# Kernel optimization log

Measured on AMD Instinct MI355X. Metric: run time of the kernel, lower is better.

Reference implementation:

```python
import jax, jax.numpy as jnp
import numpy as np

H = 128; L = 3; ODIM = 400; SCALE = 30.0

def gather_nodes(h, E_idx):
    # h: [B,N,C], E_idx: [B,N,K] -> [B,N,K,C]
    B, N, K = E_idx.shape
    C = h.shape[-1]
    idx = jnp.broadcast_to(E_idx.reshape(B, N * K, 1), (B, N * K, C))
    return jnp.take_along_axis(h, idx, axis=1).reshape(B, N, K, C)

def layer_norm(x, eps=1e-5):
    mu = jnp.mean(x, axis=-1, keepdims=True)
    var = jnp.mean((x - mu) ** 2, axis=-1, keepdims=True)
    return (x - mu) / jnp.sqrt(var + eps)

def merge_dups(h_E, inv_mapping):
    # h_E: [B,N,K,C]; inv_mapping: [B,N*K]
    B, N, K, C = h_E.shape
    flat = h_E.reshape(B, N * K, C)
    idx = jnp.broadcast_to(inv_mapping[:, :, None], (B, N * K, C))
    return jnp.take_along_axis(flat, idx, axis=1).reshape(B, N, K, C)

def setup_inputs() -> dict:
    key = jax.random.key(0)
    ks = jax.random.split(key, 40)
    B, N, K = 2, 1024, 30
    d = {}
    d['h_V0'] = jax.random.normal(ks[0], (B, N, H), jnp.float32)
    d['h_E0'] = jax.random.normal(ks[1], (B, N, K, H), jnp.float32)
    d['E_idx'] = jax.random.randint(ks[2], (B, N, K), 0, N, jnp.int32)
    d['inv_mapping'] = jax.random.randint(ks[3], (B, N * K), 0, N * K, jnp.int32)
    d['x_mask'] = jnp.ones((B, N), jnp.float32)
    s = 0.05
    d['Wv_w'] = jax.random.normal(ks[4], (H, H)) * s; d['Wv_b'] = jnp.zeros((H,))
    d['We_w'] = jax.random.normal(ks[5], (H, H)) * s; d['We_b'] = jnp.zeros((H,))
    # node MPNN layers: message MLP (3h->h->h->h) + dense FFN (h->4h->h), stacked [L,...]
    d['nW1'] = jax.random.normal(ks[6], (L, 3 * H, H)) * s; d['nb1'] = jnp.zeros((L, H))
    d['nW2'] = jax.random.normal(ks[7], (L, H, H)) * s;     d['nb2'] = jnp.zeros((L, H))
    d['nW3'] = jax.random.normal(ks[8], (L, H, H)) * s;     d['nb3'] = jnp.zeros((L, H))
    d['nWd1'] = jax.random.normal(ks[9], (L, H, 4 * H)) * s; d['nbd1'] = jnp.zeros((L, 4 * H))
    d['nWd2'] = jax.random.normal(ks[10], (L, 4 * H, H)) * s; d['nbd2'] = jnp.zeros((L, H))
    # edge MPNN layers
    d['eW1'] = jax.random.normal(ks[11], (L, 3 * H, H)) * s; d['eb1'] = jnp.zeros((L, H))
    d['eW2'] = jax.random.normal(ks[12], (L, H, H)) * s;     d['eb2'] = jnp.zeros((L, H))
    d['eW3'] = jax.random.normal(ks[13], (L, H, H)) * s;     d['eb3'] = jnp.zeros((L, H))
    d['eWd1'] = jax.random.normal(ks[14], (L, H, 4 * H)) * s; d['ebd1'] = jnp.zeros((L, 4 * H))
    d['eWd2'] = jax.random.normal(ks[15], (L, 4 * H, H)) * s; d['ebd2'] = jnp.zeros((L, H))
    d['Wout_w'] = jax.random.normal(ks[16], (H, ODIM)) * s; d['Wout_b'] = jnp.zeros((ODIM,))
    return d

def reference(h_V0, h_E0, E_idx, inv_mapping, x_mask,
              Wv_w, Wv_b, We_w, We_b,
              nW1, nb1, nW2, nb2, nW3, nb3, nWd1, nbd1, nWd2, nbd2,
              eW1, eb1, eW2, eb2, eW3, eb3, eWd1, ebd1, eWd2, ebd2,
              Wout_w, Wout_b):
    B, N, K = E_idx.shape
    h_V = h_V0 @ Wv_w + Wv_b                      # W_v embedding
    h_E = h_E0 @ We_w + We_b                      # W_e embedding
    mask_attend = gather_nodes(x_mask[..., None], E_idx)[..., 0] * x_mask[..., None]  # [B,N,K]
    for l in range(L):
        # ---- node update (NodeMPNNLayer) ----
        h_nb = gather_nodes(h_V, E_idx)                           # [B,N,K,H]
        h_i = jnp.broadcast_to(h_V[:, :, None, :], h_nb.shape)
        h_EV = jnp.concatenate([h_i, h_nb, h_E], axis=-1)         # [B,N,K,3H]
        m = jax.nn.relu(h_EV @ nW1[l] + nb1[l])
        m = jax.nn.relu(m @ nW2[l] + nb2[l])
        m = m @ nW3[l] + nb3[l]
        m = m * mask_attend[..., None]
        dh = jnp.sum(m, axis=-2) / SCALE
        h_V = layer_norm(h_V + dh)
        dh = jax.nn.relu(h_V @ nWd1[l] + nbd1[l]) @ nWd2[l] + nbd2[l]
        h_V = layer_norm(h_V + dh)
        h_V = h_V * x_mask[..., None]
        # ---- edge update (EdgeMPNNLayer) ----
        h_j = gather_nodes(h_V, E_idx)
        h_i = jnp.broadcast_to(h_V[:, :, None, :], h_j.shape)
        h_EV = jnp.concatenate([h_i, h_E, h_j], axis=-1)          # [B,N,K,3H]
        m = jax.nn.relu(h_EV @ eW1[l] + eb1[l])
        m = jax.nn.relu(m @ eW2[l] + eb2[l])
        m = m @ eW3[l] + eb3[l]
        h_E = layer_norm(h_E + m)
        dh = jax.nn.relu(h_E @ eWd1[l] + ebd1[l]) @ eWd2[l] + ebd2[l]
        h_E = layer_norm(h_E + dh)
        h_E = h_E * mask_attend[..., None]
    etab = h_E @ Wout_w + Wout_b                                  # [B,N,K,400]
    etab = merge_dups(etab, inv_mapping)
    return etab
```

## Files before the change

### kernel.cpp

```cpp
#include <hip/hip_runtime.h>
#include <hip/hip_bf16.h>
#include <stdint.h>


typedef __bf16 bf16_t;
typedef __attribute__((ext_vector_type(8))) __bf16 bf16x8;
typedef __attribute__((ext_vector_type(4))) float f32x4;

#define B_    2
#define N_    1024
#define KN    30
#define H_    128
#define L_    3
#define ODIM_ 400
#define NK    (N_ * KN)
#define RT    (B_ * N_ * KN)
#define BN_   (B_ * N_)

#define EPI_PLAIN 0
#define EPI_RELU  1
#define EPI_F32   2
#define EPI_LN    4
#define EPI_OUT   5

__device__ __forceinline__ float wred(float v) {
#pragma unroll
  for (int off = 32; off > 0; off >>= 1) v += __shfl_xor(v, off, 64);
  return v;
}

__device__ __forceinline__ void gld16(const bf16_t* g, bf16_t* l) {
  __builtin_amdgcn_global_load_lds(
      (__attribute__((address_space(1))) void*)(g),
      (__attribute__((address_space(3))) void*)(l), 16, 0, 0);
}

__device__ __forceinline__ void barL() {
  asm volatile("s_waitcnt lgkmcnt(0)" ::: "memory");
  __builtin_amdgcn_s_barrier();
  __builtin_amdgcn_sched_barrier(0);
}
__device__ __forceinline__ void wait_v4_bar() {
  asm volatile("s_waitcnt vmcnt(4) lgkmcnt(0)" ::: "memory");
  __builtin_amdgcn_s_barrier();
  __builtin_amdgcn_sched_barrier(0);
}
__device__ __forceinline__ void wait_v0_bar() {
  asm volatile("s_waitcnt vmcnt(0) lgkmcnt(0)" ::: "memory");
  __builtin_amdgcn_s_barrier();
  __builtin_amdgcn_sched_barrier(0);
}

template<int NI>
__device__ __forceinline__ void mmN(const bf16_t* __restrict__ Ah,
                                    const bf16_t* __restrict__ Bh,
                                    int wm, int wn, int fm, int q, int fx,
                                    f32x4 (&acc)[4][NI])
{
#pragma unroll
  for (int h = 0; h < 2; ++h) {
    const int slot = ((((h << 2) | q) ^ fx) << 3);
    bf16x8 af[4], bfv[NI];
#pragma unroll
    for (int mi = 0; mi < 4; ++mi)
      af[mi] = *reinterpret_cast<const bf16x8*>(
          &Ah[(wm * 64 + mi * 16 + fm) * 64 + slot]);
#pragma unroll
    for (int ni = 0; ni < NI; ++ni)
      bfv[ni] = *reinterpret_cast<const bf16x8*>(
          &Bh[(wn * (NI * 16) + ni * 16 + fm) * 64 + slot]);
#pragma unroll
    for (int mi = 0; mi < 4; ++mi)
#pragma unroll
      for (int ni = 0; ni < NI; ++ni)
        acc[mi][ni] = __builtin_amdgcn_mfma_f32_16x16x32_bf16(
            af[mi], bfv[ni], acc[mi][ni], 0, 0, 0);
  }
}

struct GCArgs {
  const bf16_t* Ain;
  const bf16_t* W1; int koff1; int ldw1;
  const bf16_t* W2; const bf16_t* b2;
  const bf16_t* W3; const bf16_t* b3;
  const float* U; const float* G; const int* E;
  const float* ma;
  float* Agg;
  const bf16_t* Wd1; const bf16_t* bd1;
  const bf16_t* Wd2; const bf16_t* bd2;
  const float* mvec;
  bf16_t* outF;
  const bf16_t* Wug; const bf16_t* bug;
  float* Uo; float* Go;
};

template<int MODE>
__global__ __launch_bounds__(256, 2) void gc(GCArgs a)
{
  __shared__ __align__(16) bf16_t bufA[2][8192];
  __shared__ __align__(16) bf16_t bufB[2][8192];
  __shared__ __align__(16) bf16_t Ws[8192];
  float* lnS  = (float*)Ws;
  float* lnS2 = lnS + 256;
  float* aggS = (float*)Ws;

  const int tid = threadIdx.x;
  const int w = tid >> 6, l = tid & 63;
  const int wm = w & 1, wn = w >> 1;
  const int row0 = blockIdx.x * 128;
  const int lr = l >> 3;
  const int kg8 = ((l & 7) ^ lr) << 3;
  const int fm = l & 15, q = l >> 4, fx = fm & 7;

  auto stage128 = [&](const bf16_t* W, int ldw, int koff) {
    const bf16_t* gb = W + (size_t)(w * 32 + lr) * ldw + koff + kg8;
#pragma unroll
    for (int s = 0; s < 4; ++s)
      gld16(gb + (size_t)(s * 8) * ldw, &Ws[w * 2048 + s * 512]);
  };
  auto stageWd1 = [&](int c) {
    const bf16_t* gb = a.Wd1 + (size_t)(c * 64 + w * 16 + lr) * 128 + kg8;
#pragma unroll
    for (int s = 0; s < 2; ++s) {
      gld16(gb + (size_t)(s * 8) * 128,      &Ws[w * 1024 + s * 512]);
      gld16(gb + (size_t)(s * 8) * 128 + 64, &Ws[4096 + w * 1024 + s * 512]);
    }
  };
  auto stageWd2 = [&](int c) {
    const bf16_t* gb = a.Wd2 + (size_t)(w * 32 + lr) * 512 + c * 64 + kg8;
#pragma unroll
    for (int s = 0; s < 4; ++s)
      gld16(gb + (size_t)(s * 8) * 512, &bufA[1][w * 2048 + s * 512]);
  };

  auto do_gemm = [&](const bf16_t* SRC, const bf16_t* W, int koff, int ldw,
                     f32x4 (&acc)[4][4]) {
#pragma unroll
    for (int kt = 0; kt < 2; ++kt) {
      __syncthreads();
      stage128(W, ldw, koff + kt * 64);
      __syncthreads();
      mmN<4>(SRC + kt * 8192, Ws, wm, wn, fm, q, fx, acc);
    }
  };

  auto wb = [&](f32x4 (&acc)[4][4], bf16_t* dst) {
#pragma unroll
    for (int mi = 0; mi < 4; ++mi)
#pragma unroll
      for (int rr = 0; rr < 4; ++rr) {
        int row = wm * 64 + mi * 16 + q * 4 + rr;
#pragma unroll
        for (int ni = 0; ni < 4; ++ni) {
          int cl = ni * 16 + fm;
          dst[wn * 8192 + row * 64 +
              ((((cl >> 3) ^ (row & 7)) << 3) | (cl & 7))] =
              (bf16_t)acc[mi][ni][rr];
        }
      }
  };

  f32x4 accA[4][4];
  auto zeroA = [&]() {
#pragma unroll
    for (int mi = 0; mi < 4; ++mi)
#pragma unroll
      for (int ni = 0; ni < 4; ++ni)
        accA[mi][ni] = f32x4{0.f, 0.f, 0.f, 0.f};
  };

  {
    bf16_t* dst = (MODE == 2) ? bufB[0] : bufA[0];
    const bf16_t* gb = a.Ain + (size_t)(row0 + w * 32 + lr) * 128 + kg8;
#pragma unroll
    for (int kt = 0; kt < 2; ++kt)
#pragma unroll
      for (int s = 0; s < 4; ++s)
        gld16(gb + (size_t)(s * 8) * 128 + kt * 64,
              dst + kt * 8192 + w * 2048 + s * 512);
  }
  if constexpr (MODE == 2) stageWd1(0);

  if constexpr (MODE <= 1) {
    zeroA();
    do_gemm(bufA[0], a.W1, a.koff1, a.ldw1, accA);
#pragma unroll
    for (int mi = 0; mi < 4; ++mi)
#pragma unroll
      for (int rr = 0; rr < 4; ++rr) {
        int rg = row0 + wm * 64 + mi * 16 + q * 4 + rr;
        const float* Ur = a.U + (size_t)(rg / KN) * 128;
        const float* Gr = a.G + (size_t)((rg / NK) * N_ + a.E[rg]) * 128;
#pragma unroll
        for (int ni = 0; ni < 4; ++ni) {
          int col = wn * 64 + ni * 16 + fm;
          accA[mi][ni][rr] = fmaxf(accA[mi][ni][rr] + Ur[col] + Gr[col], 0.f);
        }
      }
    wb(accA, bufB[0]);

    zeroA();
    do_gemm(bufB[0], a.W2, 0, 128, accA);
#pragma unroll
    for (int mi = 0; mi < 4; ++mi)
#pragma unroll
      for (int rr = 0; rr < 4; ++rr)
#pragma unroll
        for (int ni = 0; ni < 4; ++ni) {
          int col = wn * 64 + ni * 16 + fm;
          accA[mi][ni][rr] = fmaxf(accA[mi][ni][rr] + (float)a.b2[col], 0.f);
        }
    __syncthreads();
    wb(accA, bufB[0]);

    zeroA();
    do_gemm(bufB[0], a.W3, 0, 128, accA);

    if constexpr (MODE == 0) {
      __syncthreads();
      for (int i = tid; i < 768; i += 256) aggS[i] = 0.f;
      __syncthreads();
      const int nb0 = row0 / KN;
#pragma unroll
      for (int mi = 0; mi < 4; ++mi)
#pragma unroll
        for (int rr = 0; rr < 4; ++rr) {
          int rg = row0 + wm * 64 + mi * 16 + q * 4 + rr;
          float mav = a.ma[rg];
          int nl = rg / KN - nb0;
#pragma unroll
          for (int ni = 0; ni < 4; ++ni) {
            int col = wn * 64 + ni * 16 + fm;
            atomicAdd(&aggS[nl * 128 + col],
                      (accA[mi][ni][rr] + (float)a.b3[col]) * mav);
          }
        }
      __syncthreads();
      const int nbL = (row0 + 127) / KN;
      for (int i = tid; i < 768; i += 256) {
        int ng = nb0 + (i >> 7);
        if (ng <= nbL)
          atomicAdd(&a.Agg[(size_t)ng * 128 + (i & 127)], aggS[i]);
      }
      return;
    } else {
      __syncthreads();
#pragma unroll
      for (int mi = 0; mi < 4; ++mi)
#pragma unroll
        for (int rr = 0; rr < 4; ++rr) {
          int lrow = wm * 64 + mi * 16 + q * 4 + rr;
          float s = 0.f, s2 = 0.f;
#pragma unroll
          for (int ni = 0; ni < 4; ++ni) {
            int cl = ni * 16 + fm;
            float rv = (float)bufA[wn][lrow * 64 +
                ((((cl >> 3) ^ (lrow & 7)) << 3) | (cl & 7))];
            float v = accA[mi][ni][rr] + (float)a.b3[wn * 64 + cl] + rv;
            accA[mi][ni][rr] = v;
            s += v; s2 += v * v;
          }
#pragma unroll
          for (int d = 1; d < 16; d <<= 1) {
            s += __shfl_xor(s, d, 64); s2 += __shfl_xor(s2, d, 64);
          }
          if (fm == (mi * 4 + rr)) { lnS[wn * 128 + lrow] = s;
                                     lnS2[wn * 128 + lrow] = s2; }
        }
      barL();
#pragma unroll
      for (int mi = 0; mi < 4; ++mi)
#pragma unroll
        for (int rr = 0; rr < 4; ++rr) {
          int lrow = wm * 64 + mi * 16 + q * 4 + rr;
          float st = lnS[lrow] + lnS[128 + lrow];
          float st2 = lnS2[lrow] + lnS2[128 + lrow];
          float mu = st * (1.f / 128.f);
          float var = fmaxf(st2 * (1.f / 128.f) - mu * mu, 0.f);
          float rstd = rsqrtf(var + 1e-5f);
#pragma unroll
          for (int ni = 0; ni < 4; ++ni) {
            int cl = ni * 16 + fm;
            bufB[wn][lrow * 64 +
                ((((cl >> 3) ^ (lrow & 7)) << 3) | (cl & 7))] =
                (bf16_t)((accA[mi][ni][rr] - mu) * rstd);
          }
        }
      barL();
      stageWd1(0);
    }
  }

  {
    zeroA();
#pragma unroll 1
    for (int c = 0; c < 8; ++c) {
      stageWd2(c);
      wait_v4_bar();
      f32x4 accH[4][2] = {};
      __builtin_amdgcn_s_setprio(1);
      mmN<2>(bufB[0],        Ws,        wm, wn, fm, q, fx, accH);
      mmN<2>(bufB[0] + 8192, Ws + 4096, wm, wn, fm, q, fx, accH);
      __builtin_amdgcn_s_setprio(0);
#pragma unroll
      for (int mi = 0; mi < 4; ++mi)
#pragma unroll
        for (int rr = 0; rr < 4; ++rr) {
          int row = wm * 64 + mi * 16 + q * 4 + rr;
#pragma unroll
          for (int ni = 0; ni < 2; ++ni) {
            int cH = wn * 32 + ni * 16 + fm;
            float hv = fmaxf(accH[mi][ni][rr] +
                             (float)a.bd1[c * 64 + cH], 0.f);
            bufA[0][row * 64 +
                ((((cH >> 3) ^ (row & 7)) << 3) | (cH & 7))] = (bf16_t)hv;
          }
        }
      barL();
      if (c < 7) {
        stageWd1(c + 1);
        asm volatile("s_waitcnt vmcnt(4) lgkmcnt(0)" ::: "memory");
      } else {
        asm volatile("s_waitcnt vmcnt(0) lgkmcnt(0)" ::: "memory");
      }
      __builtin_amdgcn_s_barrier();
      __builtin_amdgcn_sched_barrier(0);
      __builtin_amdgcn_s_setprio(1);
      mmN<4>(bufA[0], bufA[1], wm, wn, fm, q, fx, accA);
      __builtin_amdgcn_s_setprio(0);
      __builtin_amdgcn_sched_barrier(0);
      __builtin_amdgcn_s_barrier();
      __builtin_amdgcn_sched_barrier(0);
    }

    __syncthreads();
#pragma unroll
    for (int mi = 0; mi < 4; ++mi)
#pragma unroll
      for (int rr = 0; rr < 4; ++rr) {
        int lrow = wm * 64 + mi * 16 + q * 4 + rr;
        float s = 0.f, s2 = 0.f;
#pragma unroll
        for (int ni = 0; ni < 4; ++ni) {
          int cl = ni * 16 + fm;
          float xv = (float)bufB[wn][lrow * 64 +
              ((((cl >> 3) ^ (lrow & 7)) << 3) | (cl & 7))];
          float v = accA[mi][ni][rr] + (float)a.bd2[wn * 64 + cl] + xv;
          accA[mi][ni][rr] = v;
          s += v; s2 += v * v;
        }
#pragma unroll
        for (int d = 1; d < 16; d <<= 1) {
          s += __shfl_xor(s, d, 64); s2 += __shfl_xor(s2, d, 64);
        }
        if (fm == (mi * 4 + rr)) { lnS[wn * 128 + lrow] = s;
                                   lnS2[wn * 128 + lrow] = s2; }
      }
    __syncthreads();
#pragma unroll
    for (int mi = 0; mi < 4; ++mi)
#pragma unroll
      for (int rr = 0; rr < 4; ++rr) {
        int lrow = wm * 64 + mi * 16 + q * 4 + rr;
        size_t rg = (size_t)(row0 + lrow);
        float st = lnS[lrow] + lnS[128 + lrow];
        float st2 = lnS2[lrow] + lnS2[128 + lrow];
        float mu = st * (1.f / 128.f);
        float var = fmaxf(st2 * (1.f / 128.f) - mu * mu, 0.f);
        float rstd = rsqrtf(var + 1e-5f);
        float mk = a.mvec[rg];
#pragma unroll
        for (int ni = 0; ni < 4; ++ni) {
          int col = wn * 64 + ni * 16 + fm;
          float ov = (accA[mi][ni][rr] - mu) * rstd * mk;
          a.outF[rg * 128 + col] = (bf16_t)ov;
          if constexpr (MODE == 2) accA[mi][ni][rr] = ov;
        }
      }

    if constexpr (MODE == 2) {
      __syncthreads();
      wb(accA, bufB[0]);
      zeroA();
      do_gemm(bufB[0], a.Wug, 0, 384, accA);
#pragma unroll
      for (int mi = 0; mi < 4; ++mi)
#pragma unroll
        for (int rr = 0; rr < 4; ++rr) {
          size_t rg = (size_t)(row0 + wm * 64 + mi * 16 + q * 4 + rr);
#pragma unroll
          for (int ni = 0; ni < 4; ++ni) {
            int col = wn * 64 + ni * 16 + fm;
            a.Uo[rg * 128 + col] = accA[mi][ni][rr] + (float)a.bug[col];
          }
        }
      zeroA();
      do_gemm(bufB[0], a.Wug, 256, 384, accA);
#pragma unroll
      for (int mi = 0; mi < 4; ++mi)
#pragma unroll
        for (int rr = 0; rr < 4; ++rr) {
          size_t rg = (size_t)(row0 + wm * 64 + mi * 16 + q * 4 + rr);
#pragma unroll
          for (int ni = 0; ni < 4; ++ni) {
            int col = wn * 64 + ni * 16 + fm;
            a.Go[rg * 128 + col] = accA[mi][ni][rr];
          }
        }
    }
  }
}

__global__ __launch_bounds__(256) void gk(
    const bf16_t* __restrict__ A, int lda,
    const bf16_t* __restrict__ Bt, int ldb, int koff,
    const bf16_t* __restrict__ bias,
    int N, int K, int epi,
    bf16_t* __restrict__ C,
    float* __restrict__ Cf, float* __restrict__ Cf1, int koff1,
    const float* __restrict__ U, const float* __restrict__ G,
    const int* __restrict__ E_idx,
    bf16_t* __restrict__ resid, const float* __restrict__ mvec, int row0g,
    const int* __restrict__ inv, const int* __restrict__ flag,
    void* __restrict__ outp)
{
  __shared__ __align__(16) bf16_t As[128 * 64];
  __shared__ __align__(16) bf16_t Bs[128 * 64];
  __shared__ float lnS[2][128];
  __shared__ float lnS2[2][128];

  float* CfD = Cf;
  if (epi == EPI_F32 && blockIdx.z == 1) { koff = koff1; bias = nullptr; CfD = Cf1; }

  const int tid = threadIdx.x;
  const int w = tid >> 6, l = tid & 63;
  const int wm = w & 1, wn = w >> 1;
  const int row0 = blockIdx.y * 128;
  const int col0 = blockIdx.x * 128;
  const int lr = l >> 3;
  const int kg8 = ((l & 7) ^ lr) << 3;

  const bf16_t* ap[4];
  const bf16_t* bp[4];
#pragma unroll
  for (int s = 0; s < 4; ++s) {
    int rA = row0 + w * 32 + s * 8 + lr;
    const bf16_t* abase;
    if (epi == EPI_OUT) {
      int bb = rA / NK;
      abase = A + (size_t)(bb * NK + inv[rA]) * lda;
    } else {
      abase = A + (size_t)rA * lda;
    }
    ap[s] = abase + kg8;
    int rB = col0 + w * 32 + s * 8 + lr;
    if (rB >= N) rB = N - 1;
    bp[s] = Bt + (size_t)rB * ldb + koff + kg8;
  }

  const int fm = l & 15, q = l >> 4, fx = fm & 7;
  f32x4 acc[4][4] = {};

  for (int kt = 0; kt < K; kt += 64) {
    __syncthreads();
#pragma unroll
    for (int s = 0; s < 4; ++s)
      gld16(ap[s] + kt, &As[w * 2048 + s * 512]);
#pragma unroll
    for (int s = 0; s < 4; ++s)
      gld16(bp[s] + kt, &Bs[w * 2048 + s * 512]);
    __syncthreads();
#pragma unroll
    for (int h = 0; h < 2; ++h) {
      bf16x8 af[4], bfv[4];
#pragma unroll
      for (int mi = 0; mi < 4; ++mi)
        af[mi] = *reinterpret_cast<const bf16x8*>(
            &As[(wm * 64 + mi * 16 + fm) * 64 + ((((h << 2) | q) ^ fx) << 3)]);
#pragma unroll
      for (int ni = 0; ni < 4; ++ni)
        bfv[ni] = *reinterpret_cast<const bf16x8*>(
            &Bs[(wn * 64 + ni * 16 + fm) * 64 + ((((h << 2) | q) ^ fx) << 3)]);
#pragma unroll
      for (int mi = 0; mi < 4; ++mi)
#pragma unroll
        for (int ni = 0; ni < 4; ++ni)
          acc[mi][ni] = __builtin_amdgcn_mfma_f32_16x16x32_bf16(
              af[mi], bfv[ni], acc[mi][ni], 0, 0, 0);
    }
  }

  if (epi <= EPI_F32) {
#pragma unroll
    for (int ni = 0; ni < 4; ++ni) {
      int col = col0 + wn * 64 + ni * 16 + fm;
      if (col >= N) continue;
      float bv = bias ? (float)bias[col] : 0.f;
#pragma unroll
      for (int mi = 0; mi < 4; ++mi)
#pragma unroll
        for (int rr = 0; rr < 4; ++rr) {
          size_t rg = (size_t)(row0g + row0 + wm * 64 + mi * 16 + q * 4 + rr);
          float v = acc[mi][ni][rr] + bv;
          if (epi == EPI_RELU) v = fmaxf(v, 0.f);
          if (epi == EPI_F32) CfD[rg * N + col] = v;
          else                C[rg * N + col] = (bf16_t)v;
        }
    }
  } else if (epi == EPI_LN) {
#pragma unroll
    for (int mi = 0; mi < 4; ++mi)
#pragma unroll
      for (int rr = 0; rr < 4; ++rr) {
        int lrow = wm * 64 + mi * 16 + q * 4 + rr;
        size_t rg = (size_t)(row0g + row0 + lrow);
        float s = 0.f, s2 = 0.f;
#pragma unroll
        for (int ni = 0; ni < 4; ++ni) {
          int col = wn * 64 + ni * 16 + fm;
          float v = acc[mi][ni][rr] + (bias ? (float)bias[col] : 0.f)
                    + (float)resid[rg * 128 + col];
          acc[mi][ni][rr] = v;
          s += v; s2 += v * v;
        }
#pragma unroll
        for (int d = 1; d < 16; d <<= 1) {
          s += __shfl_xor(s, d, 64); s2 += __shfl_xor(s2, d, 64);
        }
        if (fm == (mi * 4 + rr)) { lnS[wn][lrow] = s; lnS2[wn][lrow] = s2; }
      }
    __syncthreads();
#pragma unroll
    for (int mi = 0; mi < 4; ++mi)
#pragma unroll
      for (int rr = 0; rr < 4; ++rr) {
        int lrow = wm * 64 + mi * 16 + q * 4 + rr;
        size_t rg = (size_t)(row0g + row0 + lrow);
        float st = lnS[0][lrow] + lnS[1][lrow];
        float st2 = lnS2[0][lrow] + lnS2[1][lrow];
        float mu = st * (1.f / 128.f);
        float var = fmaxf(st2 * (1.f / 128.f) - mu * mu, 0.f);
        float rstd = rsqrtf(var + 1e-5f);
        float mk = mvec ? mvec[rg] : 1.f;
#pragma unroll
        for (int ni = 0; ni < 4; ++ni) {
          int col = wn * 64 + ni * 16 + fm;
          resid[rg * 128 + col] = (bf16_t)((acc[mi][ni][rr] - mu) * rstd * mk);
        }
      }
  } else if (epi == EPI_OUT) {
    const int fl = *flag;
#pragma unroll
    for (int ni = 0; ni < 4; ++ni) {
      int col = col0 + wn * 64 + ni * 16 + fm;
      if (col >= ODIM_) continue;
      float bv = bias ? (float)bias[col] : 0.f;
#pragma unroll
      for (int mi = 0; mi < 4; ++mi)
#pragma unroll
        for (int rr = 0; rr < 4; ++rr) {
          size_t rg = (size_t)(row0 + wm * 64 + mi * 16 + q * 4 + rr);
          float v = acc[mi][ni][rr] + bv;
          size_t idx = rg * ODIM_ + col;
          if (fl) ((bf16_t*)outp)[idx] = (bf16_t)v;
          else    ((float*)outp)[idx]  = v;
        }
    }
  }
}

__global__ void flag_kernel(const uint32_t* __restrict__ xm_raw,
                            int* __restrict__ flag)
{
  if (threadIdx.x == 0 && blockIdx.x == 0)
    *flag = (xm_raw[0] == 0x3F803F80u) ? 1 : 0;
}

struct ConvSeg { const void* src; void* dst; int n; int K; int N; };
struct ConvArgs { ConvSeg s[29]; };

__global__ __launch_bounds__(256) void conv_kernel(
    ConvArgs a, int nseg, int total8, const int* __restrict__ flag)
{
  int t = blockIdx.x * 256 + threadIdx.x;
  if (t >= total8) return;
  const int fl = *flag;
  int seg = 0, t8 = t;
  while (seg < nseg - 1 && t8 >= (a.s[seg].n >> 3)) { t8 -= a.s[seg].n >> 3; ++seg; }
  const ConvSeg sg = a.s[seg];
  const int e = t8 << 3;
  float vals[8];
  if (fl) {
    union { uint4 v; bf16_t b[8]; } u;
    u.v = *((const uint4*)sg.src + t8);
#pragma unroll
    for (int j = 0; j < 8; ++j) vals[j] = (float)u.b[j];
  } else {
    const float* sp = (const float*)sg.src + e;
#pragma unroll
    for (int j = 0; j < 8; ++j) vals[j] = sp[j];
  }
  if (sg.N == 0) {
    union { uint4 v; bf16_t b[8]; } o;
#pragma unroll
    for (int j = 0; j < 8; ++j) o.b[j] = (bf16_t)vals[j];
    *((uint4*)sg.dst + t8) = o.v;
  } else {
    const int KN_ = sg.K * sg.N;
    const int lay = e / KN_;
    const int rem = e - lay * KN_;
    const int k = rem / sg.N;
    const int n0 = rem - k * sg.N;
    bf16_t* dp = (bf16_t*)sg.dst + (size_t)lay * KN_ + k;
#pragma unroll
    for (int j = 0; j < 8; ++j)
      dp[(size_t)(n0 + j) * sg.K] = (bf16_t)vals[j];
  }
}

__global__ __launch_bounds__(256) void mask_kernel(
    const bf16_t* __restrict__ xm, const int* __restrict__ E_idx,
    float* __restrict__ ma, float* __restrict__ xmf)
{
  int r = blockIdx.x * 256 + threadIdx.x;
  if (r >= RT) return;
  if (r < BN_) xmf[r] = (float)xm[r];
  int b = r / NK;
  int n = (r / KN) % N_;
  ma[r] = (float)xm[b * N_ + E_idx[r]] * (float)xm[b * N_ + n];
}

__global__ __launch_bounds__(256) void zero_kernel(float* __restrict__ p, int n)
{
  int i = blockIdx.x * 256 + threadIdx.x;
  if (i < n) p[i] = 0.f;
}

__global__ __launch_bounds__(128) void node_ln_kernel(
    float* __restrict__ Agg, bf16_t* __restrict__ hV)
{
  int bn = blockIdx.x;
  int c = threadIdx.x;
  size_t idx = (size_t)bn * H_ + c;
  float v = (float)hV[idx] + Agg[idx] * (1.0f / 30.0f);
  Agg[idx] = 0.f;
  __shared__ float red[4];
  float ss = wred(v), s2 = wred(v * v);
  int w = c >> 6, lane = c & 63;
  if (lane == 0) { red[w * 2] = ss; red[w * 2 + 1] = s2; }
  __syncthreads();
  float tot = red[0] + red[2], tot2 = red[1] + red[3];
  float mu = tot * (1.f / 128.f);
  float var = fmaxf(tot2 * (1.f / 128.f) - mu * mu, 0.f);
  float rstd = rsqrtf(var + 1e-5f);
  hV[idx] = (bf16_t)((v - mu) * rstd);
}

extern "C" void kernel_launch(void* const* d_in, const int* in_sizes, int n_in,
                              void* d_out, int out_size, void* d_ws, size_t ws_size,
                              hipStream_t stream)
{
  const int* E_idx  = (const int*)d_in[2];
  const int* invmap = (const int*)d_in[3];

  char* ws = (char*)d_ws;
  size_t woff = 0;
  auto walloc = [&](size_t bytes) -> char* {
    char* p = ws + woff; woff += (bytes + 255) & ~(size_t)255; return p;
  };
  int*    flag  = (int*)walloc(4);
  bf16_t* WtOut = (bf16_t*)walloc((size_t)51200 * 2);
  bf16_t* outbc = (bf16_t*)walloc((size_t)400 * 2);
  bf16_t* hE    = (bf16_t*)walloc((size_t)RT * H_ * 2);

  char* ob = (char*)d_out;
  bf16_t* t0 = (bf16_t*)ob;
  bf16_t* t1 = (bf16_t*)(ob + (size_t)RT * H_ * 2);
  size_t ooff = (size_t)RT * H_ * 2 * 2;
  auto oalloc = [&](size_t bytes) -> char* {
    char* p = ob + ooff; ooff += (bytes + 255) & ~(size_t)255; return p;
  };
  bf16_t* WtV  = (bf16_t*)oalloc(16384 * 2);
  bf16_t* bvc  = (bf16_t*)oalloc(128 * 2);
  bf16_t* WtE  = (bf16_t*)oalloc(16384 * 2);
  bf16_t* bec  = (bf16_t*)oalloc(128 * 2);
  bf16_t* Wtn1 = (bf16_t*)oalloc((size_t)147456 * 2);
  bf16_t* nb1c = (bf16_t*)oalloc(384 * 2);
  bf16_t* Wtn2 = (bf16_t*)oalloc((size_t)49152 * 2);
  bf16_t* nb2c = (bf16_t*)oalloc(384 * 2);
  bf16_t* Wtn3 = (bf16_t*)oalloc((size_t)49152 * 2);
  bf16_t* nb3c = (bf16_t*)oalloc(384 * 2);
  bf16_t* Wtnd1 = (bf16_t*)oalloc((size_t)196608 * 2);
  bf16_t* nbd1c = (bf16_t*)oalloc(1536 * 2);
  bf16_t* Wtnd2 = (bf16_t*)oalloc((size_t)196608 * 2);
  bf16_t* nbd2c = (bf16_t*)oalloc(384 * 2);
  bf16_t* Wte1 = (bf16_t*)oalloc((size_t)147456 * 2);
  bf16_t* eb1c = (bf16_t*)oalloc(384 * 2);
  bf16_t* Wte2 = (bf16_t*)oalloc((size_t)49152 * 2);
  bf16_t* eb2c = (bf16_t*)oalloc(384 * 2);
  bf16_t* Wte3 = (bf16_t*)oalloc((size_t)49152 * 2);
  bf16_t* eb3c = (bf16_t*)oalloc(384 * 2);
  bf16_t* Wted1 = (bf16_t*)oalloc((size_t)196608 * 2);
  bf16_t* ebd1c = (bf16_t*)oalloc(1536 * 2);
  bf16_t* Wted2 = (bf16_t*)oalloc((size_t)196608 * 2);
  bf16_t* ebd2c = (bf16_t*)oalloc(384 * 2);
  float*  Ubuf = (float*)oalloc((size_t)BN_ * 128 * 4);
  float*  Gbuf = (float*)oalloc((size_t)BN_ * 128 * 4);
  bf16_t* hV   = (bf16_t*)oalloc((size_t)BN_ * 128 * 2);
  float*  ma   = (float*)oalloc((size_t)RT * 4);
  bf16_t* xm   = (bf16_t*)oalloc((size_t)BN_ * 2);
  float*  xmf  = (float*)oalloc((size_t)BN_ * 4);
  float*  Abuf = (float*)oalloc((size_t)BN_ * 128 * 4);

  ConvArgs ca;
  struct D { int idx; void* dst; int K; int N; };
  const D dl[29] = {
    {0, t1, 0, 0}, {1, t0, 0, 0}, {4, xm, 0, 0},
    {5, WtV, 128, 128}, {6, bvc, 0, 0}, {7, WtE, 128, 128}, {8, bec, 0, 0},
    {9, Wtn1, 384, 128}, {10, nb1c, 0, 0}, {11, Wtn2, 128, 128}, {12, nb2c, 0, 0},
    {13, Wtn3, 128, 128}, {14, nb3c, 0, 0},
    {15, Wtnd1, 128, 512}, {16, nbd1c, 0, 0}, {17, Wtnd2, 512, 128}, {18, nbd2c, 0, 0},
    {19, Wte1, 384, 128}, {20, eb1c, 0, 0}, {21, Wte2, 128, 128}, {22, eb2c, 0, 0},
    {23, Wte3, 128, 128}, {24, eb3c, 0, 0},
    {25, Wted1, 128, 512}, {26, ebd1c, 0, 0}, {27, Wted2, 512, 128}, {28, ebd2c, 0, 0},
    {29, WtOut, 128, 400}, {30, outbc, 0, 0}
  };
  int total8 = 0;
  for (int i = 0; i < 29; ++i) {
    ca.s[i].src = d_in[dl[i].idx];
    ca.s[i].dst = dl[i].dst;
    ca.s[i].n   = in_sizes[dl[i].idx];
    ca.s[i].K   = dl[i].K;
    ca.s[i].N   = dl[i].N;
    total8 += ca.s[i].n >> 3;
  }

  auto g = [&](dim3 grid, const bf16_t* A, int lda, const bf16_t* Bt, int ldb,
               int koff, const bf16_t* bias, int N, int K, int epi,
               bf16_t* C, float* Cf, float* Cf1, int koff1,
               bf16_t* resid, const float* mvec, int row0g) {
    gk<<<grid, 256, 0, stream>>>(A, lda, Bt, ldb, koff, bias, N, K, epi,
        C, Cf, Cf1, koff1, Ubuf, Gbuf, E_idx, resid, mvec, row0g,
        invmap, flag, d_out);
  };
  const float* NOM = nullptr;

  flag_kernel<<<1, 64, 0, stream>>>((const uint32_t*)d_in[4], flag);
  conv_kernel<<<(total8 + 255) / 256, 256, 0, stream>>>(ca, 29, total8, flag);
  mask_kernel<<<RT / 256, 256, 0, stream>>>(xm, E_idx, ma, xmf);
  zero_kernel<<<(BN_ * 128) / 256, 256, 0, stream>>>(Abuf, BN_ * 128);

  g(dim3(1, BN_ / 128), t1, 128, WtV, 128, 0, bvc, 128, 128, EPI_PLAIN,
    hV, nullptr, nullptr, 0, nullptr, NOM, 0);
  g(dim3(1, RT / 128), t0, 128, WtE, 128, 0, bec, 128, 128, EPI_PLAIN,
    hE, nullptr, nullptr, 0, nullptr, NOM, 0);

  for (int l = 0; l < L_; ++l) {
    g(dim3(1, BN_ / 128, 2), hV, 128, Wtn1 + (size_t)l * 49152, 384, 0,
      nb1c + l * 128, 128, 128, EPI_F32,
      nullptr, Ubuf, Gbuf, 128, nullptr, NOM, 0);
    {
      GCArgs na{};
      na.Ain = hE;
      na.W1 = Wtn1 + (size_t)l * 49152; na.koff1 = 256; na.ldw1 = 384;
      na.W2 = Wtn2 + (size_t)l * 16384; na.b2 = nb2c + l * 128;
      na.W3 = Wtn3 + (size_t)l * 16384; na.b3 = nb3c + l * 128;
      na.U = Ubuf; na.G = Gbuf; na.E = E_idx;
      na.ma = ma; na.Agg = Abuf;
      gc<0><<<RT / 128, 256, 0, stream>>>(na);
    }
    node_ln_kernel<<<BN_, 128, 0, stream>>>(Abuf, hV);
    {
      GCArgs nf{};
      nf.Ain = hV;
      nf.Wd1 = Wtnd1 + (size_t)l * 65536; nf.bd1 = nbd1c + l * 512;
      nf.Wd2 = Wtnd2 + (size_t)l * 65536; nf.bd2 = nbd2c + l * 128;
      nf.mvec = xmf; nf.outF = hV;
      nf.Wug = Wte1 + (size_t)l * 49152; nf.bug = eb1c + l * 128;
      nf.Uo = Ubuf; nf.Go = Gbuf;
      gc<2><<<BN_ / 128, 256, 0, stream>>>(nf);
    }
    {
      GCArgs ea{};
      ea.Ain = hE;
      ea.W1 = Wte1 + (size_t)l * 49152; ea.koff1 = 128; ea.ldw1 = 384;
      ea.W2 = Wte2 + (size_t)l * 16384; ea.b2 = eb2c + l * 128;
      ea.W3 = Wte3 + (size_t)l * 16384; ea.b3 = eb3c + l * 128;
      ea.U = Ubuf; ea.G = Gbuf; ea.E = E_idx;
      ea.Wd1 = Wted1 + (size_t)l * 65536; ea.bd1 = ebd1c + l * 512;
      ea.Wd2 = Wted2 + (size_t)l * 65536; ea.bd2 = ebd2c + l * 128;
      ea.mvec = ma; ea.outF = hE;
      gc<1><<<RT / 128, 256, 0, stream>>>(ea);
    }
  }

  g(dim3(4, RT / 128), hE, 128, WtOut, 128, 0, outbc, ODIM_, 128, EPI_OUT,
    nullptr, nullptr, nullptr, 0, nullptr, NOM, 0);
}
```

Before: 701.1 us.

## Split node FFN across hidden-dim chunks with partial sums and separate LN

Replaces the single fused node-FFN kernel (gc<2>), which ran only 16 blocks, with a kernel that splits the 512-wide hidden dimension into 8 chunks, giving 128 blocks. Each block writes fp32 partial outputs to a scratch buffer. A separate kernel sums the partials, adds the residual and applies layernorm and the mask. The edge U/G projection is recomputed by the generic GEMM kernel. This raises parallelism on the small node path, at the cost of two extra launches and extra global traffic for the partials.

```diff
diff --git a/kernel.cpp b/kernel.cpp
--- a/kernel.cpp
+++ b/kernel.cpp
@@ -42,11 +42,6 @@
 }
 __device__ __forceinline__ void wait_v4_bar() {
   asm volatile("s_waitcnt vmcnt(4) lgkmcnt(0)" ::: "memory");
-  __builtin_amdgcn_s_barrier();
-  __builtin_amdgcn_sched_barrier(0);
-}
-__device__ __forceinline__ void wait_v0_bar() {
-  asm volatile("s_waitcnt vmcnt(0) lgkmcnt(0)" ::: "memory");
   __builtin_amdgcn_s_barrier();
   __builtin_amdgcn_sched_barrier(0);
 }
@@ -90,8 +85,6 @@
   const bf16_t* Wd2; const bf16_t* bd2;
   const float* mvec;
   bf16_t* outF;
-  const bf16_t* Wug; const bf16_t* bug;
-  float* Uo; float* Go;
 };
 
 template<int MODE>
@@ -170,128 +163,122 @@
   };
 
   {
-    bf16_t* dst = (MODE == 2) ? bufB[0] : bufA[0];
     const bf16_t* gb = a.Ain + (size_t)(row0 + w * 32 + lr) * 128 + kg8;
 #pragma unroll
     for (int kt = 0; kt < 2; ++kt)
 #pragma unroll
       for (int s = 0; s < 4; ++s)
         gld16(gb + (size_t)(s * 8) * 128 + kt * 64,
-              dst + kt * 8192 + w * 2048 + s * 512);
-  }
-  if constexpr (MODE == 2) stageWd1(0);
-
-  if constexpr (MODE <= 1) {
-    zeroA();
-    do_gemm(bufA[0], a.W1, a.koff1, a.ldw1, accA);
+              bufA[0] + kt * 8192 + w * 2048 + s * 512);
+  }
+
+  zeroA();
+  do_gemm(bufA[0], a.W1, a.koff1, a.ldw1, accA);
+#pragma unroll
+  for (int mi = 0; mi < 4; ++mi)
+#pragma unroll
+    for (int rr = 0; rr < 4; ++rr) {
+      int rg = row0 + wm * 64 + mi * 16 + q * 4 + rr;
+      const float* Ur = a.U + (size_t)(rg / KN) * 128;
+      const float* Gr = a.G + (size_t)((rg / NK) * N_ + a.E[rg]) * 128;
+#pragma unroll
+      for (int ni = 0; ni < 4; ++ni) {
+        int col = wn * 64 + ni * 16 + fm;
+        accA[mi][ni][rr] = fmaxf(accA[mi][ni][rr] + Ur[col] + Gr[col], 0.f);
+      }
+    }
+  wb(accA, bufB[0]);
+
+  zeroA();
+  do_gemm(bufB[0], a.W2, 0, 128, accA);
+#pragma unroll
+  for (int mi = 0; mi < 4; ++mi)
+#pragma unroll
+    for (int rr = 0; rr < 4; ++rr)
+#pragma unroll
+      for (int ni = 0; ni < 4; ++ni) {
+        int col = wn * 64 + ni * 16 + fm;
+        accA[mi][ni][rr] = fmaxf(accA[mi][ni][rr] + (float)a.b2[col], 0.f);
+      }
+  __syncthreads();
+  wb(accA, bufB[0]);
+
+  zeroA();
+  do_gemm(bufB[0], a.W3, 0, 128, accA);
+
+  if constexpr (MODE == 0) {
+    __syncthreads();
+    for (int i = tid; i < 768; i += 256) aggS[i] = 0.f;
+    __syncthreads();
+    const int nb0 = row0 / KN;
 #pragma unroll
     for (int mi = 0; mi < 4; ++mi)
 #pragma unroll
       for (int rr = 0; rr < 4; ++rr) {
         int rg = row0 + wm * 64 + mi * 16 + q * 4 + rr;
-        const float* Ur = a.U + (size_t)(rg / KN) * 128;
-        const float* Gr = a.G + (size_t)((rg / NK) * N_ + a.E[rg]) * 128;
+        float mav = a.ma[rg];
+        int nl = rg / KN - nb0;
 #pragma unroll
         for (int ni = 0; ni < 4; ++ni) {
           int col = wn * 64 + ni * 16 + fm;
-          accA[mi][ni][rr] = fmaxf(accA[mi][ni][rr] + Ur[col] + Gr[col], 0.f);
-        }
-      }
-    wb(accA, bufB[0]);
-
-    zeroA();
-    do_gemm(bufB[0], a.W2, 0, 128, accA);
-#pragma unroll
-    for (int mi = 0; mi < 4; ++mi)
-#pragma unroll
-      for (int rr = 0; rr < 4; ++rr)
+          atomicAdd(&aggS[nl * 128 + col],
+                    (accA[mi][ni][rr] + (float)a.b3[col]) * mav);
+        }
+      }
+    __syncthreads();
+    const int nbL = (row0 + 127) / KN;
+    for (int i = tid; i < 768; i += 256) {
+      int ng = nb0 + (i >> 7);
+      if (ng <= nbL)
+        atomicAdd(&a.Agg[(size_t)ng * 128 + (i & 127)], aggS[i]);
+    }
+    return;
+  } else {
+    __syncthreads();
+#pragma unroll
+    for (int mi = 0; mi < 4; ++mi)
+#pragma unroll
+      for (int rr = 0; rr < 4; ++rr) {
+        int lrow = wm * 64 + mi * 16 + q * 4 + rr;
+        float s = 0.f, s2 = 0.f;
 #pragma unroll
         for (int ni = 0; ni < 4; ++ni) {
-          int col = wn * 64 + ni * 16 + fm;
-          accA[mi][ni][rr] = fmaxf(accA[mi][ni][rr] + (float)a.b2[col], 0.f);
-        }
-    __syncthreads();
-    wb(accA, bufB[0]);
-
-    zeroA();
-    do_gemm(bufB[0], a.W3, 0, 128, accA);
-
-    if constexpr (MODE == 0) {
-      __syncthreads();
-      for (int i = tid; i < 768; i += 256) aggS[i] = 0.f;
-      __syncthreads();
-      const int nb0 = row0 / KN;
-#pragma unroll
-      for (int mi = 0; mi < 4; ++mi)
-#pragma unroll
-        for (int rr = 0; rr < 4; ++rr) {
-          int rg = row0 + wm * 64 + mi * 16 + q * 4 + rr;
-          float mav = a.ma[rg];
-          int nl = rg / KN - nb0;
-#pragma unroll
-          for (int ni = 0; ni < 4; ++ni) {
-            int col = wn * 64 + ni * 16 + fm;
-            atomicAdd(&aggS[nl * 128 + col],
-                      (accA[mi][ni][rr] + (float)a.b3[col]) * mav);
-          }
-        }
-      __syncthreads();
-      const int nbL = (row0 + 127) / KN;
-      for (int i = tid; i < 768; i += 256) {
-        int ng = nb0 + (i >> 7);
-        if (ng <= nbL)
-          atomicAdd(&a.Agg[(size_t)ng * 128 + (i & 127)], aggS[i]);
-      }
-      return;
-    } else {
-      __syncthreads();
-#pragma unroll
-      for (int mi = 0; mi < 4; ++mi)
-#pragma unroll
-        for (int rr = 0; rr < 4; ++rr) {
-          int lrow = wm * 64 + mi * 16 + q * 4 + rr;
-          float s = 0.f, s2 = 0.f;
-#pragma unroll
-          for (int ni = 0; ni < 4; ++ni) {
-            int cl = ni * 16 + fm;
-            float rv = (float)bufA[wn][lrow * 64 +
-                ((((cl >> 3) ^ (lrow & 7)) << 3) | (cl & 7))];
-            float v = accA[mi][ni][rr] + (float)a.b3[wn * 64 + cl] + rv;
-            accA[mi][ni][rr] = v;
-            s += v; s2 += v * v;
-          }
-#pragma unroll
-          for (int d = 1; d < 16; d <<= 1) {
-            s += __shfl_xor(s, d, 64); s2 += __shfl_xor(s2, d, 64);
-          }
-          if (fm == (mi * 4 + rr)) { lnS[wn * 128 + lrow] = s;
-                                     lnS2[wn * 128 + lrow] = s2; }
-        }
-      barL();
-#pragma unroll
-      for (int mi = 0; mi < 4; ++mi)
-#pragma unroll
-        for (int rr = 0; rr < 4; ++rr) {
-          int lrow = wm * 64 + mi * 16 + q * 4 + rr;
-          float st = lnS[lrow] + lnS[128 + lrow];
-          float st2 = lnS2[lrow] + lnS2[128 + lrow];
-          float mu = st * (1.f / 128.f);
-          float var = fmaxf(st2 * (1.f / 128.f) - mu * mu, 0.f);
-          float rstd = rsqrtf(var + 1e-5f);
-#pragma unroll
-          for (int ni = 0; ni < 4; ++ni) {
-            int cl = ni * 16 + fm;
-            bufB[wn][lrow * 64 +
-                ((((cl >> 3) ^ (lrow & 7)) << 3) | (cl & 7))] =
-                (bf16_t)((accA[mi][ni][rr] - mu) * rstd);
-          }
-        }
-      barL();
-      stageWd1(0);
-    }
-  }
-
-  {
+          int cl = ni * 16 + fm;
+          float rv = (float)bufA[wn][lrow * 64 +
+              ((((cl >> 3) ^ (lrow & 7)) << 3) | (cl & 7))];
+          float v = accA[mi][ni][rr] + (float)a.b3[wn * 64 + cl] + rv;
+          accA[mi][ni][rr] = v;
+          s += v; s2 += v * v;
+        }
+#pragma unroll
+        for (int d = 1; d < 16; d <<= 1) {
+          s += __shfl_xor(s, d, 64); s2 += __shfl_xor(s2, d, 64);
+        }
+        if (fm == (mi * 4 + rr)) { lnS[wn * 128 + lrow] = s;
+                                   lnS2[wn * 128 + lrow] = s2; }
+      }
+    barL();
+#pragma unroll
+    for (int mi = 0; mi < 4; ++mi)
+#pragma unroll
+      for (int rr = 0; rr < 4; ++rr) {
+        int lrow = wm * 64 + mi * 16 + q * 4 + rr;
+        float st = lnS[lrow] + lnS[128 + lrow];
+        float st2 = lnS2[lrow] + lnS2[128 + lrow];
+        float mu = st * (1.f / 128.f);
+        float var = fmaxf(st2 * (1.f / 128.f) - mu * mu, 0.f);
+        float rstd = rsqrtf(var + 1e-5f);
+#pragma unroll
+        for (int ni = 0; ni < 4; ++ni) {
+          int cl = ni * 16 + fm;
+          bufB[wn][lrow * 64 +
+              ((((cl >> 3) ^ (lrow & 7)) << 3) | (cl & 7))] =
+              (bf16_t)((accA[mi][ni][rr] - mu) * rstd);
+        }
+      }
+    barL();
+    stageWd1(0);
+
     zeroA();
 #pragma unroll 1
     for (int c = 0; c < 8; ++c) {
@@ -372,43 +359,113 @@
 #pragma unroll
         for (int ni = 0; ni < 4; ++ni) {
           int col = wn * 64 + ni * 16 + fm;
-          float ov = (accA[mi][ni][rr] - mu) * rstd * mk;
-          a.outF[rg * 128 + col] = (bf16_t)ov;
-          if constexpr (MODE == 2) accA[mi][ni][rr] = ov;
-        }
-      }
-
-    if constexpr (MODE == 2) {
-      __syncthreads();
-      wb(accA, bufB[0]);
-      zeroA();
-      do_gemm(bufB[0], a.Wug, 0, 384, accA);
-#pragma unroll
-      for (int mi = 0; mi < 4; ++mi)
-#pragma unroll
-        for (int rr = 0; rr < 4; ++rr) {
-          size_t rg = (size_t)(row0 + wm * 64 + mi * 16 + q * 4 + rr);
-#pragma unroll
-          for (int ni = 0; ni < 4; ++ni) {
-            int col = wn * 64 + ni * 16 + fm;
-            a.Uo[rg * 128 + col] = accA[mi][ni][rr] + (float)a.bug[col];
-          }
-        }
-      zeroA();
-      do_gemm(bufB[0], a.Wug, 256, 384, accA);
-#pragma unroll
-      for (int mi = 0; mi < 4; ++mi)
-#pragma unroll
-        for (int rr = 0; rr < 4; ++rr) {
-          size_t rg = (size_t)(row0 + wm * 64 + mi * 16 + q * 4 + rr);
-#pragma unroll
-          for (int ni = 0; ni < 4; ++ni) {
-            int col = wn * 64 + ni * 16 + fm;
-            a.Go[rg * 128 + col] = accA[mi][ni][rr];
-          }
-        }
-    }
-  }
+          a.outF[rg * 128 + col] = (bf16_t)((accA[mi][ni][rr] - mu) * rstd * mk);
+        }
+      }
+  }
+}
+
+__global__ __launch_bounds__(256, 2) void gf(
+    const bf16_t* __restrict__ X,
+    const bf16_t* __restrict__ Wd1,
+    const bf16_t* __restrict__ bd1,
+    const bf16_t* __restrict__ Wd2,
+    float* __restrict__ Fp)
+{
+  __shared__ __align__(16) bf16_t Xs[2][8192];
+  __shared__ __align__(16) bf16_t W1s[2][4096];
+  __shared__ __align__(16) bf16_t Hs[8192];
+  __shared__ __align__(16) bf16_t W2s[8192];
+
+  const int c = blockIdx.x;
+  const int row0 = blockIdx.y * 128;
+  const int tid = threadIdx.x;
+  const int w = tid >> 6, l = tid & 63;
+  const int wm = w & 1, wn = w >> 1;
+  const int lr = l >> 3;
+  const int kg8 = ((l & 7) ^ lr) << 3;
+  const int fm = l & 15, q = l >> 4, fx = fm & 7;
+
+  {
+    const bf16_t* gb = X + (size_t)(row0 + w * 32 + lr) * 128 + kg8;
+#pragma unroll
+    for (int kt = 0; kt < 2; ++kt)
+#pragma unroll
+      for (int s = 0; s < 4; ++s)
+        gld16(gb + (size_t)(s * 8) * 128 + kt * 64,
+              Xs[0] + kt * 8192 + w * 2048 + s * 512);
+  }
+  {
+    const bf16_t* gb = Wd1 + (size_t)(c * 64 + w * 16 + lr) * 128 + kg8;
+#pragma unroll
+    for (int s = 0; s < 2; ++s) {
+      gld16(gb + (size_t)(s * 8) * 128,      &W1s[0][w * 1024 + s * 512]);
+      gld16(gb + (size_t)(s * 8) * 128 + 64, &W1s[1][w * 1024 + s * 512]);
+    }
+  }
+  {
+    const bf16_t* gb = Wd2 + (size_t)(w * 32 + lr) * 512 + c * 64 + kg8;
+#pragma unroll
+    for (int s = 0; s < 4; ++s)
+      gld16(gb + (size_t)(s * 8) * 512, &W2s[w * 2048 + s * 512]);
+  }
+  __syncthreads();
+
+  f32x4 accH[4][2] = {};
+  mmN<2>(Xs[0],        W1s[0], wm, wn, fm, q, fx, accH);
+  mmN<2>(Xs[0] + 8192, W1s[1], wm, wn, fm, q, fx, accH);
+#pragma unroll
+  for (int mi = 0; mi < 4; ++mi)
+#pragma unroll
+    for (int rr = 0; rr < 4; ++rr) {
+      int row = wm * 64 + mi * 16 + q * 4 + rr;
+#pragma unroll
+      for (int ni = 0; ni < 2; ++ni) {
+        int cH = wn * 32 + ni * 16 + fm;
+        float hv = fmaxf(accH[mi][ni][rr] + (float)bd1[c * 64 + cH], 0.f);
+        Hs[row * 64 + ((((cH >> 3) ^ (row & 7)) << 3) | (cH & 7))] =
+            (bf16_t)hv;
+      }
+    }
+  barL();
+
+  f32x4 accF[4][4] = {};
+  mmN<4>(Hs, W2s, wm, wn, fm, q, fx, accF);
+  float* out = Fp + ((size_t)c * BN_ + row0) * 128;
+#pragma unroll
+  for (int mi = 0; mi < 4; ++mi)
+#pragma unroll
+    for (int rr = 0; rr < 4; ++rr) {
+      int row = wm * 64 + mi * 16 + q * 4 + rr;
+#pragma unroll
+      for (int ni = 0; ni < 4; ++ni) {
+        int col = wn * 64 + ni * 16 + fm;
+        out[(size_t)row * 128 + col] = accF[mi][ni][rr];
+      }
+    }
+}
+
+__global__ __launch_bounds__(128) void ffn_ln_kernel(
+    const float* __restrict__ Fp, const bf16_t* __restrict__ bd2,
+    const float* __restrict__ xmf, bf16_t* __restrict__ hV)
+{
+  int bn = blockIdx.x;
+  int c = threadIdx.x;
+  size_t idx = (size_t)bn * H_ + c;
+  float f = 0.f;
+#pragma unroll
+  for (int k = 0; k < 8; ++k) f += Fp[(size_t)k * BN_ * H_ + idx];
+  float v = (float)hV[idx] + f + (float)bd2[c];
+  __shared__ float red[4];
+  float ss = wred(v), s2 = wred(v * v);
+  int w = c >> 6, lane = c & 63;
+  if (lane == 0) { red[w * 2] = ss; red[w * 2 + 1] = s2; }
+  __syncthreads();
+  float tot = red[0] + red[2], tot2 = red[1] + red[3];
+  float mu = tot * (1.f / 128.f);
+  float var = fmaxf(tot2 * (1.f / 128.f) - mu * mu, 0.f);
+  float rstd = rsqrtf(var + 1e-5f);
+  hV[idx] = (bf16_t)((v - mu) * rstd * xmf[bn]);
 }
 
 __global__ __launch_bounds__(256) void gk(
@@ -676,6 +733,7 @@
   char* ob = (char*)d_out;
   bf16_t* t0 = (bf16_t*)ob;
   bf16_t* t1 = (bf16_t*)(ob + (size_t)RT * H_ * 2);
+  float*  Fpart = (float*)t0;
   size_t ooff = (size_t)RT * H_ * 2 * 2;
   auto oalloc = [&](size_t bytes) -> char* {
     char* p = ob + ooff; ooff += (bytes + 255) & ~(size_t)255; return p;
@@ -770,16 +828,13 @@
       gc<0><<<RT / 128, 256, 0, stream>>>(na);
     }
     node_ln_kernel<<<BN_, 128, 0, stream>>>(Abuf, hV);
-    {
-      GCArgs nf{};
-      nf.Ain = hV;
-      nf.Wd1 = Wtnd1 + (size_t)l * 65536; nf.bd1 = nbd1c + l * 512;
-      nf.Wd2 = Wtnd2 + (size_t)l * 65536; nf.bd2 = nbd2c + l * 128;
-      nf.mvec = xmf; nf.outF = hV;
-      nf.Wug = Wte1 + (size_t)l * 49152; nf.bug = eb1c + l * 128;
-      nf.Uo = Ubuf; nf.Go = Gbuf;
-      gc<2><<<BN_ / 128, 256, 0, stream>>>(nf);
-    }
+    gf<<<dim3(8, BN_ / 128), 256, 0, stream>>>(
+        hV, Wtnd1 + (size_t)l * 65536, nbd1c + l * 512,
+        Wtnd2 + (size_t)l * 65536, Fpart);
+    ffn_ln_kernel<<<BN_, 128, 0, stream>>>(Fpart, nbd2c + l * 128, xmf, hV);
+    g(dim3(1, BN_ / 128, 2), hV, 128, Wte1 + (size_t)l * 49152, 384, 0,
+      eb1c + l * 128, 128, 128, EPI_F32,
+      nullptr, Ubuf, Gbuf, 256, nullptr, NOM, 0);
     {
       GCArgs ea{};
       ea.Ain = hE;
```

After: 733.3 us. 4.6% more time.
